# Performance work log

Hardware: AMD Instinct MI355X
Metric: run time of the kernel (lower is better)

Reference implementation:

```python
import jax, jax.numpy as jnp
import numpy as np

B, T, HID = 4, 2048, 2048
N_HEAD, N_KV, HD = 16, 2, 128
N_REP = N_HEAD // N_KV


def setup_inputs() -> dict:
    key = jax.random.key(0)
    ks = jax.random.split(key, 7)
    s = 0.02
    return {
        "x": jax.random.normal(ks[0], (B, T, HID), jnp.float32),
        "cos": jax.random.normal(ks[1], (T, 1, HD // 2), jnp.float32),
        "sin": jax.random.normal(ks[2], (T, 1, HD // 2), jnp.float32),
        "Wq": jax.random.normal(ks[3], (N_HEAD * HD, HID), jnp.float32) * s,
        "Wk": jax.random.normal(ks[4], (N_KV * HD, HID), jnp.float32) * s,
        "Wv": jax.random.normal(ks[5], (N_KV * HD, HID), jnp.float32) * s,
        "Wo": jax.random.normal(ks[6], (HID, HID), jnp.float32) * s,
    }


def _rope(x, cos, sin):
    # x: (B, T, H, HD); cos/sin: (T, 1, HD//2) broadcast over B and H
    x_r = x[..., 0::2]
    x_i = x[..., 1::2]
    out_r = x_r * cos - x_i * sin
    out_i = x_r * sin + x_i * cos
    return jnp.stack([out_r, out_i], axis=-1).reshape(x.shape)


def _rms_norm(x):
    eps = jnp.finfo(x.dtype).eps
    var = jnp.mean(jnp.square(x), axis=-1, keepdims=True)
    return x * jax.lax.rsqrt(var + eps)


def reference(x, cos, sin, Wq, Wk, Wv, Wo):
    b, t, _ = x.shape
    q = (x @ Wq.T).reshape(b, t, N_HEAD, HD)
    k = (x @ Wk.T).reshape(b, t, N_KV, HD)
    v = (x @ Wv.T).reshape(b, t, N_KV, HD)
    q = _rms_norm(_rope(q, cos, sin))
    k = _rms_norm(_rope(k, cos, sin))
    # GQA without materializing repeated K/V: group q heads per kv head
    # q: (b, t, n_kv, n_rep, hd) -> (b, n_kv, n_rep, t, hd)
    q = q.reshape(b, t, N_KV, N_REP, HD).transpose(0, 2, 3, 1, 4)
    k = k.transpose(0, 2, 1, 3)  # (b, n_kv, t, hd)
    v = v.transpose(0, 2, 1, 3)
    scale = 1.0 / jnp.sqrt(jnp.asarray(HD, x.dtype))
    scores = jnp.einsum("bgrtd,bgsd->bgrts", q, k) * scale
    causal = jnp.tril(jnp.ones((t, t), dtype=bool))
    scores = jnp.where(causal, scores, jnp.asarray(-jnp.inf, scores.dtype))
    attn = jax.nn.softmax(scores, axis=-1)
    y = jnp.einsum("bgrts,bgsd->bgrtd", attn, v)
    # (b, n_kv, n_rep, t, hd) -> (b, t, n_head*hd)
    y = y.transpose(0, 3, 1, 2, 4).reshape(b, t, N_HEAD * HD)
    return y @ Wo.T
```

## Files before the change

### kernel.cpp

```cpp
#include <hip/hip_runtime.h>

#define B_    4
#define T_    2048
#define HID_  2048
#define NH_   16
#define NKV_  2
#define HD_   128
#define M_    (B_ * T_)
#define NQKV_ 2560

typedef __bf16 bf16x8 __attribute__((ext_vector_type(8)));
typedef float  f32x4  __attribute__((ext_vector_type(4)));

#define AS1 __attribute__((address_space(1)))
#define AS3 __attribute__((address_space(3)))

#if __has_builtin(__builtin_amdgcn_exp2f)
#define EXP2(x) __builtin_amdgcn_exp2f(x)
#else
#define EXP2(x) exp2f(x)
#endif

__device__ __forceinline__ void load_lds16(const void* g, void* l) {
  __builtin_amdgcn_global_load_lds((const AS1 unsigned int*)g,
                                   (AS3 unsigned int*)l, 16, 0, 0);
}

__device__ __forceinline__ unsigned short f2bf(float x) {
  union { float f; unsigned u; } a; a.f = x;
  unsigned r = a.u + 0x7fffu + ((a.u >> 16) & 1u);
  return (unsigned short)(r >> 16);
}
__device__ __forceinline__ float bf2f(unsigned h) {
  union { unsigned u; float f; } a; a.u = h << 16;
  return a.f;
}
__device__ __forceinline__ unsigned pk_rtz(float lo, float hi) {
  union { float f; unsigned u; } a, b; a.f = lo; b.f = hi;
  return (a.u >> 16) | (b.u & 0xffff0000u);
}

__global__ __launch_bounds__(256) void cast_bf16(const float* __restrict__ in,
                                                 unsigned short* __restrict__ out,
                                                 int n4) {
  int i = blockIdx.x * 256 + threadIdx.x;
  if (i >= n4) return;
  float4 v = ((const float4*)in)[i];
  ushort4 o;
  o.x = f2bf(v.x); o.y = f2bf(v.y); o.z = f2bf(v.z); o.w = f2bf(v.w);
  ((ushort4*)out)[i] = o;
}

__global__ __launch_bounds__(256) void cast_w(const float* __restrict__ Wq,
                                              const float* __restrict__ Wk,
                                              const float* __restrict__ Wv,
                                              unsigned short* __restrict__ out) {
  int i = blockIdx.x * 256 + threadIdx.x;
  const float* src; int j;
  if (i < 1048576)      { src = Wq; j = i; }
  else if (i < 1179648) { src = Wk; j = i - 1048576; }
  else                  { src = Wv; j = i - 1179648; }
  float4 v = ((const float4*)src)[j];
  ushort4 o;
  o.x = f2bf(v.x); o.y = f2bf(v.y); o.z = f2bf(v.z); o.w = f2bf(v.w);
  ((ushort4*)out)[i] = o;
}

template <int OUT_BF16>
__global__ __launch_bounds__(256) void gemm_bt(const unsigned short* __restrict__ A,
                                               const unsigned short* __restrict__ Bm,
                                               void* __restrict__ C,
                                               int M, int N, int K) {
  __shared__ __align__(16) unsigned short As[128 * 32];
  __shared__ __align__(16) unsigned short Bs[128 * 32];
  const int tid = threadIdx.x;
  const int w = tid >> 6, lane = tid & 63;
  const int m0 = blockIdx.y << 7, n0 = blockIdx.x << 7;
  const int c = lane & 15, grp = lane >> 4;
  const int lr = lane >> 2;
  const int su = (((lane & 3) ^ ((lr >> 1) & 3)) << 3);
  const int sw = (c >> 1) & 3;
  const int wm = (w & 1) << 6, wn = (w >> 1) << 6;
  f32x4 acc[4][4] = {};
  for (int k0 = 0; k0 < K; k0 += 32) {
    __syncthreads();
    {
      int r0 = w << 4;
      load_lds16(A + (size_t)(m0 + r0 + lr) * K + k0 + su, &As[r0 * 32]);
      load_lds16(A + (size_t)(m0 + 64 + r0 + lr) * K + k0 + su, &As[(64 + r0) * 32]);
      load_lds16(Bm + (size_t)(n0 + r0 + lr) * K + k0 + su, &Bs[r0 * 32]);
      load_lds16(Bm + (size_t)(n0 + 64 + r0 + lr) * K + k0 + su, &Bs[(64 + r0) * 32]);
    }
    __syncthreads();
    bf16x8 af[4], bf[4];
#pragma unroll
    for (int i = 0; i < 4; i++)
      af[i] = *(const bf16x8*)&As[(wm + i * 16 + c) * 32 + ((grp ^ sw) << 3)];
#pragma unroll
    for (int j = 0; j < 4; j++)
      bf[j] = *(const bf16x8*)&Bs[(wn + j * 16 + c) * 32 + ((grp ^ sw) << 3)];
#pragma unroll
    for (int i = 0; i < 4; i++)
#pragma unroll
      for (int j = 0; j < 4; j++)
        acc[i][j] = __builtin_amdgcn_mfma_f32_16x16x32_bf16(af[i], bf[j], acc[i][j], 0, 0, 0);
  }
#pragma unroll
  for (int i = 0; i < 4; i++)
#pragma unroll
    for (int j = 0; j < 4; j++)
#pragma unroll
      for (int r = 0; r < 4; r++) {
        int row = m0 + wm + i * 16 + grp * 4 + r;
        int col = n0 + wn + j * 16 + c;
        float v = acc[i][j][r];
        if (OUT_BF16) ((unsigned short*)C)[(size_t)row * N + col] = f2bf(v);
        else          ((float*)C)[(size_t)row * N + col] = v;
      }
}

__global__ __launch_bounds__(256) void rope_norm(const unsigned short* __restrict__ qkv,
                                                 const float* __restrict__ cosb,
                                                 const float* __restrict__ sinb,
                                                 unsigned short* __restrict__ qo,
                                                 unsigned short* __restrict__ ko,
                                                 unsigned short* __restrict__ vo) {
  const int m = blockIdx.x;
  const int b = m >> 11, t = m & 2047;
  const int w = threadIdx.x >> 6, lane = threadIdx.x & 63;
  const float cv = cosb[t * 64 + lane], sv = sinb[t * 64 + lane];
  const unsigned short* row = qkv + (size_t)m * NQKV_;
  const float QSCL = 0.08838834764831845f * 1.4426950408889634f;
  for (int hh = w; hh < 20; hh += 4) {
    if (hh < 18) {
      const int col0 = (hh < 16) ? hh * 128 : 2048 + (hh - 16) * 128;
      unsigned pr = *(const unsigned*)(row + col0 + 2 * lane);
      float xr = bf2f(pr & 0xffffu), xi = bf2f(pr >> 16);
      float orr = xr * cv - xi * sv;
      float oi  = xr * sv + xi * cv;
      float ss = orr * orr + oi * oi;
#pragma unroll
      for (int off = 1; off < 64; off <<= 1) ss += __shfl_xor(ss, off);
      float scl = rsqrtf(ss * (1.0f / 128.0f) + 1.1920929e-07f);
      if (hh < 16) {
        float s2 = scl * QSCL;
        unsigned out = (unsigned)f2bf(orr * s2) | ((unsigned)f2bf(oi * s2) << 16);
        *(unsigned*)(qo + (((size_t)(b * NH_ + hh)) * T_ + t) * HD_ + 2 * lane) = out;
      } else {
        unsigned out = (unsigned)f2bf(orr * scl) | ((unsigned)f2bf(oi * scl) << 16);
        *(unsigned*)(ko + (((size_t)(b * NKV_ + (hh - 16))) * T_ + t) * HD_ + 2 * lane) = out;
      }
    } else {
      const int gg = hh - 18;
      unsigned pr = *(const unsigned*)(row + 2304 + gg * 128 + 2 * lane);
      *(unsigned*)(vo + (((size_t)(b * NKV_ + gg)) * T_ + t) * HD_ + 2 * lane) = pr;
    }
  }
}

__global__ __launch_bounds__(256) void transpose_v(const unsigned short* __restrict__ v,
                                                   unsigned short* __restrict__ vt) {
  __shared__ unsigned short tile[64][65];
  const int bg = blockIdx.z;
  const int t0 = blockIdx.x << 6, h0 = blockIdx.y << 6;
  const unsigned short* src = v + (size_t)bg * T_ * HD_;
  unsigned short* dst = vt + (size_t)bg * T_ * HD_;
  const int tid = threadIdx.x;
  const int rr = tid >> 4, cc = (tid & 15) << 2;
  const int u = (cc >> 2) & 7;
  const int cp = (cc & 32) + 16 * (u & 1) + 4 * ((u >> 1) & 3);
#pragma unroll
  for (int it = 0; it < 4; it++) {
    int r = rr + it * 16;
    ushort4 d = *(const ushort4*)(src + (size_t)(t0 + r) * HD_ + h0 + cc);
    tile[r][cc + 0] = d.x; tile[r][cc + 1] = d.y;
    tile[r][cc + 2] = d.z; tile[r][cc + 3] = d.w;
  }
  __syncthreads();
#pragma unroll
  for (int it = 0; it < 4; it++) {
    int r = rr + it * 16;
    ushort4 d;
    d.x = tile[cp + 0][r]; d.y = tile[cp + 1][r];
    d.z = tile[cp + 2][r]; d.w = tile[cp + 3][r];
    *(ushort4*)(dst + (size_t)(h0 + r) * T_ + t0 + cc) = d;
  }
}

__global__ __launch_bounds__(256, 2) void flash_attn(const unsigned short* __restrict__ q,
                                                     const unsigned short* __restrict__ k,
                                                     const unsigned short* __restrict__ vt,
                                                     unsigned short* __restrict__ y) {
  __shared__ __align__(16) unsigned short Kb[2][8192];
  __shared__ __align__(16) unsigned short Vb[2][8192];
  const int tid = threadIdx.x;
  const int w = tid >> 6, lane = tid & 63;
  const int c = lane & 15, grp = lane >> 4;
  const int lr = lane >> 2;
  const int sw = (c >> 1) & 3;
  const int su = (((lane & 3) ^ ((lr >> 1) & 3)) << 3);
  const int t0 = (15 - (int)blockIdx.x) << 7;
  const int t0w = t0 + w * 32;
  const int hq = blockIdx.y, b = blockIdx.z, g = hq >> 3;
  const unsigned short* qbase = q + (((size_t)(b * NH_ + hq)) * T_ + t0) * HD_;
  const unsigned short* kbase = k + ((size_t)(b * NKV_ + g)) * T_ * HD_;
  const unsigned short* vtbase = vt + ((size_t)(b * NKV_ + g)) * HD_ * T_;

  bf16x8 qf[2][4];
#pragma unroll
  for (int ti = 0; ti < 2; ti++)
#pragma unroll
    for (int ks = 0; ks < 4; ks++)
      qf[ti][ks] = *(const bf16x8*)(qbase + (size_t)(w * 32 + ti * 16 + c) * HD_ + ks * 32 + grp * 8);

  f32x4 oacc[2][8] = {};
  float mrun[2], lrun[2];
  mrun[0] = mrun[1] = -__builtin_inff();
  lrun[0] = lrun[1] = 0.f;

  auto stage = [&](int s0, int bb) {
    const unsigned short* kp = kbase + (size_t)(s0 + w * 16 + lr) * HD_ + su;
#pragma unroll
    for (int dc = 0; dc < 4; dc++)
      load_lds16(kp + dc * 32, &Kb[bb][dc * 2048 + (w * 16) * 32]);
    const unsigned short* vp = vtbase + s0 + su;
#pragma unroll
    for (int ks = 0; ks < 2; ks++)
#pragma unroll
      for (int jj = 0; jj < 2; jj++)
        load_lds16(vp + (size_t)(w * 32 + jj * 16 + lr) * T_ + ks * 32,
                   &Vb[bb][ks * 4096 + (w * 32 + jj * 16) * 32]);
  };

  const int nch = (t0 >> 6) + 2;
  stage(0, 0);
  __syncthreads();
  for (int ic = 0; ic < nch; ic++) {
    const int s0 = ic << 6, bb = ic & 1;
    if (ic + 1 < nch) stage((ic + 1) << 6, bb ^ 1);
    if (s0 <= t0w + 31) {
      const unsigned short* Kc = Kb[bb];
      const unsigned short* Vc = Vb[bb];
      f32x4 st[2][4] = {};
#pragma unroll
      for (int s = 0; s < 4; s++)
#pragma unroll
        for (int kvt = 0; kvt < 4; kvt++) {
          bf16x8 ak = *(const bf16x8*)&Kc[s * 2048 + (kvt * 16 + c) * 32 + ((grp ^ sw) << 3)];
          st[0][kvt] = __builtin_amdgcn_mfma_f32_16x16x32_bf16(ak, qf[0][s], st[0][kvt], 0, 0, 0);
          st[1][kvt] = __builtin_amdgcn_mfma_f32_16x16x32_bf16(ak, qf[1][s], st[1][kvt], 0, 0, 0);
        }
      if (s0 + 63 > t0w) {
#pragma unroll
        for (int ti = 0; ti < 2; ti++)
#pragma unroll
          for (int kvt = 0; kvt < 4; kvt++)
#pragma unroll
            for (int r = 0; r < 4; r++) {
              int kv = s0 + kvt * 16 + grp * 4 + r;
              int qq = t0w + ti * 16 + c;
              if (kv > qq) st[ti][kvt][r] = -__builtin_inff();
            }
      }
      unsigned pkv[2][4][2];
#pragma unroll
      for (int ti = 0; ti < 2; ti++) {
        float rm = st[ti][0][0];
#pragma unroll
        for (int kvt = 0; kvt < 4; kvt++)
#pragma unroll
          for (int r = 0; r < 4; r++) rm = fmaxf(rm, st[ti][kvt][r]);
        rm = fmaxf(rm, __shfl_xor(rm, 16));
        rm = fmaxf(rm, __shfl_xor(rm, 32));
        float mnew = fmaxf(mrun[ti], rm);
        float alpha = EXP2(mrun[ti] - mnew);
        mrun[ti] = mnew;
        float rs = 0.f;
#pragma unroll
        for (int kvt = 0; kvt < 4; kvt++) {
          float p0 = EXP2(st[ti][kvt][0] - mnew);
          float p1 = EXP2(st[ti][kvt][1] - mnew);
          float p2 = EXP2(st[ti][kvt][2] - mnew);
          float p3 = EXP2(st[ti][kvt][3] - mnew);
          rs += (p0 + p1) + (p2 + p3);
          pkv[ti][kvt][0] = pk_rtz(p0, p1);
          pkv[ti][kvt][1] = pk_rtz(p2, p3);
        }
        rs += __shfl_xor(rs, 16);
        rs += __shfl_xor(rs, 32);
        lrun[ti] = lrun[ti] * alpha + rs;
#pragma unroll
        for (int hj = 0; hj < 8; hj++)
#pragma unroll
          for (int r = 0; r < 4; r++) oacc[ti][hj][r] *= alpha;
      }
#pragma unroll
      for (int s = 0; s < 2; s++) {
        union { int4 i; bf16x8 v; } pf0, pf1;
        pf0.i = make_int4(pkv[0][2 * s][0], pkv[0][2 * s][1], pkv[0][2 * s + 1][0], pkv[0][2 * s + 1][1]);
        pf1.i = make_int4(pkv[1][2 * s][0], pkv[1][2 * s][1], pkv[1][2 * s + 1][0], pkv[1][2 * s + 1][1]);
#pragma unroll
        for (int hj = 0; hj < 8; hj++) {
          union { int4 i; bf16x8 v; } av;
          av.i = *(const int4*)&Vc[s * 4096 + (hj * 16 + c) * 32 + ((grp ^ sw) << 3)];
          oacc[0][hj] = __builtin_amdgcn_mfma_f32_16x16x32_bf16(av.v, pf0.v, oacc[0][hj], 0, 0, 0);
          oacc[1][hj] = __builtin_amdgcn_mfma_f32_16x16x32_bf16(av.v, pf1.v, oacc[1][hj], 0, 0, 0);
        }
      }
    }
    __syncthreads();
  }

#pragma unroll
  for (int ti = 0; ti < 2; ti++) {
    float inv = 1.f / lrun[ti];
    int trow = t0 + w * 32 + ti * 16 + c;
#pragma unroll
    for (int hj = 0; hj < 8; hj++) {
      ushort4 o;
      o.x = f2bf(oacc[ti][hj][0] * inv);
      o.y = f2bf(oacc[ti][hj][1] * inv);
      o.z = f2bf(oacc[ti][hj][2] * inv);
      o.w = f2bf(oacc[ti][hj][3] * inv);
      *(ushort4*)&y[((size_t)(b * T_ + trow)) * HID_ + hq * HD_ + hj * 16 + grp * 4] = o;
    }
  }
}

extern "C" void kernel_launch(void* const* d_in, const int* in_sizes, int n_in,
                              void* d_out, int out_size, void* d_ws, size_t ws_size,
                              hipStream_t stream) {
  const float* x    = (const float*)d_in[0];
  const float* cosb = (const float*)d_in[1];
  const float* sinb = (const float*)d_in[2];
  const float* Wq   = (const float*)d_in[3];
  const float* Wk   = (const float*)d_in[4];
  const float* Wv   = (const float*)d_in[5];
  const float* Wo   = (const float*)d_in[6];
  float* out = (float*)d_out;

  char* ws = (char*)d_ws;
  size_t off = 0;
  auto take = [&](size_t elems) {
    unsigned short* p = (unsigned short*)(ws + off);
    off += ((elems * 2 + 255) & ~(size_t)255);
    return p;
  };
  unsigned short* xb   = take((size_t)M_ * HID_);
  unsigned short* wqkv = take((size_t)NQKV_ * HID_);
  unsigned short* wob  = take((size_t)HID_ * HID_);
  unsigned short* qkv  = take((size_t)M_ * NQKV_);
  unsigned short* qb   = take((size_t)B_ * NH_ * T_ * HD_);
  unsigned short* kb   = take((size_t)B_ * NKV_ * T_ * HD_);
  unsigned short* vb   = take((size_t)B_ * NKV_ * T_ * HD_);
  unsigned short* vtb  = take((size_t)B_ * NKV_ * T_ * HD_);
  unsigned short* yb   = take((size_t)M_ * HID_);
  (void)ws_size; (void)in_sizes; (void)n_in; (void)out_size;

  cast_bf16<<<16384, 256, 0, stream>>>(x, xb, 4194304);
  cast_w<<<5120, 256, 0, stream>>>(Wq, Wk, Wv, wqkv);
  cast_bf16<<<4096, 256, 0, stream>>>(Wo, wob, 1048576);

  gemm_bt<1><<<dim3(20, 64), 256, 0, stream>>>(xb, wqkv, qkv, M_, NQKV_, HID_);
  rope_norm<<<8192, 256, 0, stream>>>(qkv, cosb, sinb, qb, kb, vb);
  transpose_v<<<dim3(32, 2, 8), 256, 0, stream>>>(vb, vtb);
  flash_attn<<<dim3(16, 16, 4), 256, 0, stream>>>(qb, kb, vtb, yb);
  gemm_bt<0><<<dim3(16, 64), 256, 0, stream>>>(yb, wob, out, M_, HID_, HID_);
}
```

Before: 546.3 us.

## Load V directly from global, drop V LDS staging, remap block schedule

```diff
diff --git a/kernel.cpp b/kernel.cpp
--- a/kernel.cpp
+++ b/kernel.cpp
@@ -187,24 +187,32 @@
   }
 }
 
-__global__ __launch_bounds__(256, 2) void flash_attn(const unsigned short* __restrict__ q,
+__global__ __launch_bounds__(256, 4) void flash_attn(const unsigned short* __restrict__ q,
                                                      const unsigned short* __restrict__ k,
                                                      const unsigned short* __restrict__ vt,
                                                      unsigned short* __restrict__ y) {
   __shared__ __align__(16) unsigned short Kb[2][8192];
-  __shared__ __align__(16) unsigned short Vb[2][8192];
   const int tid = threadIdx.x;
   const int w = tid >> 6, lane = tid & 63;
   const int c = lane & 15, grp = lane >> 4;
   const int lr = lane >> 2;
   const int sw = (c >> 1) & 3;
   const int su = (((lane & 3) ^ ((lr >> 1) & 3)) << 3);
-  const int t0 = (15 - (int)blockIdx.x) << 7;
+
+  const int idx = blockIdx.x;
+  const int j = idx >> 8;
+  const int u = idx & 15;
+  const int v = (idx >> 4) & 15;
+  const int tp = (u + 2 * (j >> 1)) & 15;
+  const int tile_i = (j & 1) ? tp : (15 - tp);
+  const int t0 = tile_i << 7;
+  const int hq = v, b = j, g = hq >> 3;
   const int t0w = t0 + w * 32;
-  const int hq = blockIdx.y, b = blockIdx.z, g = hq >> 3;
+
   const unsigned short* qbase = q + (((size_t)(b * NH_ + hq)) * T_ + t0) * HD_;
   const unsigned short* kbase = k + ((size_t)(b * NKV_ + g)) * T_ * HD_;
   const unsigned short* vtbase = vt + ((size_t)(b * NKV_ + g)) * HD_ * T_;
+  const unsigned short* vg = vtbase + (size_t)c * T_ + grp * 8;
 
   bf16x8 qf[2][4];
 #pragma unroll
@@ -223,13 +231,6 @@
 #pragma unroll
     for (int dc = 0; dc < 4; dc++)
       load_lds16(kp + dc * 32, &Kb[bb][dc * 2048 + (w * 16) * 32]);
-    const unsigned short* vp = vtbase + s0 + su;
-#pragma unroll
-    for (int ks = 0; ks < 2; ks++)
-#pragma unroll
-      for (int jj = 0; jj < 2; jj++)
-        load_lds16(vp + (size_t)(w * 32 + jj * 16 + lr) * T_ + ks * 32,
-                   &Vb[bb][ks * 4096 + (w * 32 + jj * 16) * 32]);
   };
 
   const int nch = (t0 >> 6) + 2;
@@ -240,7 +241,6 @@
     if (ic + 1 < nch) stage((ic + 1) << 6, bb ^ 1);
     if (s0 <= t0w + 31) {
       const unsigned short* Kc = Kb[bb];
-      const unsigned short* Vc = Vb[bb];
       f32x4 st[2][4] = {};
 #pragma unroll
       for (int s = 0; s < 4; s++)
@@ -296,15 +296,17 @@
       }
 #pragma unroll
       for (int s = 0; s < 2; s++) {
+        union { int4 i; bf16x8 v; } av[8];
+#pragma unroll
+        for (int hj = 0; hj < 8; hj++)
+          av[hj].i = *(const int4*)(vg + (size_t)(hj * 16) * T_ + s0 + s * 32);
         union { int4 i; bf16x8 v; } pf0, pf1;
         pf0.i = make_int4(pkv[0][2 * s][0], pkv[0][2 * s][1], pkv[0][2 * s + 1][0], pkv[0][2 * s + 1][1]);
         pf1.i = make_int4(pkv[1][2 * s][0], pkv[1][2 * s][1], pkv[1][2 * s + 1][0], pkv[1][2 * s + 1][1]);
 #pragma unroll
         for (int hj = 0; hj < 8; hj++) {
-          union { int4 i; bf16x8 v; } av;
-          av.i = *(const int4*)&Vc[s * 4096 + (hj * 16 + c) * 32 + ((grp ^ sw) << 3)];
-          oacc[0][hj] = __builtin_amdgcn_mfma_f32_16x16x32_bf16(av.v, pf0.v, oacc[0][hj], 0, 0, 0);
-          oacc[1][hj] = __builtin_amdgcn_mfma_f32_16x16x32_bf16(av.v, pf1.v, oacc[1][hj], 0, 0, 0);
+          oacc[0][hj] = __builtin_amdgcn_mfma_f32_16x16x32_bf16(av[hj].v, pf0.v, oacc[0][hj], 0, 0, 0);
+          oacc[1][hj] = __builtin_amdgcn_mfma_f32_16x16x32_bf16(av[hj].v, pf1.v, oacc[1][hj], 0, 0, 0);
         }
       }
     }
@@ -364,6 +366,6 @@
   gemm_bt<1><<<dim3(20, 64), 256, 0, stream>>>(xb, wqkv, qkv, M_, NQKV_, HID_);
   rope_norm<<<8192, 256, 0, stream>>>(qkv, cosb, sinb, qb, kb, vb);
   transpose_v<<<dim3(32, 2, 8), 256, 0, stream>>>(vb, vtb);
-  flash_attn<<<dim3(16, 16, 4), 256, 0, stream>>>(qb, kb, vtb, yb);
+  flash_attn<<<dim3(1024), 256, 0, stream>>>(qb, kb, vtb, yb);
   gemm_bt<0><<<dim3(16, 64), 256, 0, stream>>>(yb, wob, out, M_, HID_, HID_);
 }
```

New measurement: 768.1 us. 40.6% more time.

## Pair causal tiles per block, skip small rescales, raise MFMA priority

Applied to the files above, without the earlier changes.

```diff
diff --git a/kernel.cpp b/kernel.cpp
--- a/kernel.cpp
+++ b/kernel.cpp
@@ -199,24 +199,15 @@
   const int lr = lane >> 2;
   const int sw = (c >> 1) & 3;
   const int su = (((lane & 3) ^ ((lr >> 1) & 3)) << 3);
-  const int t0 = (15 - (int)blockIdx.x) << 7;
-  const int t0w = t0 + w * 32;
-  const int hq = blockIdx.y, b = blockIdx.z, g = hq >> 3;
-  const unsigned short* qbase = q + (((size_t)(b * NH_ + hq)) * T_ + t0) * HD_;
-  const unsigned short* kbase = k + ((size_t)(b * NKV_ + g)) * T_ * HD_;
+
+  const int idx = blockIdx.x;
+  const int p  = idx & 7;
+  const int hq = (idx >> 3) & 15;
+  const int b  = idx >> 7;
+  const int g  = hq >> 3;
+
+  const unsigned short* kbase  = k  + ((size_t)(b * NKV_ + g)) * T_ * HD_;
   const unsigned short* vtbase = vt + ((size_t)(b * NKV_ + g)) * HD_ * T_;
-
-  bf16x8 qf[2][4];
-#pragma unroll
-  for (int ti = 0; ti < 2; ti++)
-#pragma unroll
-    for (int ks = 0; ks < 4; ks++)
-      qf[ti][ks] = *(const bf16x8*)(qbase + (size_t)(w * 32 + ti * 16 + c) * HD_ + ks * 32 + grp * 8);
-
-  f32x4 oacc[2][8] = {};
-  float mrun[2], lrun[2];
-  mrun[0] = mrun[1] = -__builtin_inff();
-  lrun[0] = lrun[1] = 0.f;
 
   auto stage = [&](int s0, int bb) {
     const unsigned short* kp = kbase + (size_t)(s0 + w * 16 + lr) * HD_ + su;
@@ -232,97 +223,124 @@
                    &Vb[bb][ks * 4096 + (w * 32 + jj * 16) * 32]);
   };
 
-  const int nch = (t0 >> 6) + 2;
-  stage(0, 0);
-  __syncthreads();
-  for (int ic = 0; ic < nch; ic++) {
-    const int s0 = ic << 6, bb = ic & 1;
-    if (ic + 1 < nch) stage((ic + 1) << 6, bb ^ 1);
-    if (s0 <= t0w + 31) {
-      const unsigned short* Kc = Kb[bb];
-      const unsigned short* Vc = Vb[bb];
-      f32x4 st[2][4] = {};
-#pragma unroll
-      for (int s = 0; s < 4; s++)
-#pragma unroll
-        for (int kvt = 0; kvt < 4; kvt++) {
-          bf16x8 ak = *(const bf16x8*)&Kc[s * 2048 + (kvt * 16 + c) * 32 + ((grp ^ sw) << 3)];
-          st[0][kvt] = __builtin_amdgcn_mfma_f32_16x16x32_bf16(ak, qf[0][s], st[0][kvt], 0, 0, 0);
-          st[1][kvt] = __builtin_amdgcn_mfma_f32_16x16x32_bf16(ak, qf[1][s], st[1][kvt], 0, 0, 0);
+  for (int ph = 0; ph < 2; ph++) {
+    const int tile = ph ? p : (15 - p);
+    const int t0 = tile << 7;
+    const int t0w = t0 + w * 32;
+    const unsigned short* qbase = q + (((size_t)(b * NH_ + hq)) * T_ + t0) * HD_;
+
+    bf16x8 qf[2][4];
+#pragma unroll
+    for (int ti = 0; ti < 2; ti++)
+#pragma unroll
+      for (int ks = 0; ks < 4; ks++)
+        qf[ti][ks] = *(const bf16x8*)(qbase + (size_t)(w * 32 + ti * 16 + c) * HD_ + ks * 32 + grp * 8);
+
+    f32x4 oacc[2][8] = {};
+    float mrun[2], lrun[2];
+    mrun[0] = mrun[1] = -__builtin_inff();
+    lrun[0] = lrun[1] = 0.f;
+
+    const int nch = (t0 >> 6) + 2;
+    stage(0, 0);
+    __syncthreads();
+    for (int ic = 0; ic < nch; ic++) {
+      const int s0 = ic << 6, bb = ic & 1;
+      if (ic + 1 < nch) stage((ic + 1) << 6, bb ^ 1);
+      if (s0 <= t0w + 31) {
+        const unsigned short* Kc = Kb[bb];
+        const unsigned short* Vc = Vb[bb];
+        f32x4 st[2][4] = {};
+        __builtin_amdgcn_s_setprio(1);
+#pragma unroll
+        for (int s = 0; s < 4; s++)
+#pragma unroll
+          for (int kvt = 0; kvt < 4; kvt++) {
+            bf16x8 ak = *(const bf16x8*)&Kc[s * 2048 + (kvt * 16 + c) * 32 + ((grp ^ sw) << 3)];
+            st[0][kvt] = __builtin_amdgcn_mfma_f32_16x16x32_bf16(ak, qf[0][s], st[0][kvt], 0, 0, 0);
+            st[1][kvt] = __builtin_amdgcn_mfma_f32_16x16x32_bf16(ak, qf[1][s], st[1][kvt], 0, 0, 0);
+          }
+        __builtin_amdgcn_s_setprio(0);
+        if (s0 + 63 > t0w) {
+#pragma unroll
+          for (int ti = 0; ti < 2; ti++)
+#pragma unroll
+            for (int kvt = 0; kvt < 4; kvt++)
+#pragma unroll
+              for (int r = 0; r < 4; r++) {
+                int kv = s0 + kvt * 16 + grp * 4 + r;
+                int qq = t0w + ti * 16 + c;
+                if (kv > qq) st[ti][kvt][r] = -__builtin_inff();
+              }
         }
-      if (s0 + 63 > t0w) {
-#pragma unroll
-        for (int ti = 0; ti < 2; ti++)
+        unsigned pkv[2][4][2];
+#pragma unroll
+        for (int ti = 0; ti < 2; ti++) {
+          float rm = st[ti][0][0];
 #pragma unroll
           for (int kvt = 0; kvt < 4; kvt++)
 #pragma unroll
-            for (int r = 0; r < 4; r++) {
-              int kv = s0 + kvt * 16 + grp * 4 + r;
-              int qq = t0w + ti * 16 + c;
-              if (kv > qq) st[ti][kvt][r] = -__builtin_inff();
-            }
+            for (int r = 0; r < 4; r++) rm = fmaxf(rm, st[ti][kvt][r]);
+          rm = fmaxf(rm, __shfl_xor(rm, 16));
+          rm = fmaxf(rm, __shfl_xor(rm, 32));
+          if (!__all(rm <= mrun[ti] + 8.f)) {
+            float mnew = fmaxf(mrun[ti], rm);
+            float alpha = EXP2(mrun[ti] - mnew);
+            mrun[ti] = mnew;
+            lrun[ti] *= alpha;
+#pragma unroll
+            for (int hj = 0; hj < 8; hj++)
+#pragma unroll
+              for (int r = 0; r < 4; r++) oacc[ti][hj][r] *= alpha;
+          }
+          const float m0 = mrun[ti];
+          float rs = 0.f;
+#pragma unroll
+          for (int kvt = 0; kvt < 4; kvt++) {
+            float p0 = EXP2(st[ti][kvt][0] - m0);
+            float p1 = EXP2(st[ti][kvt][1] - m0);
+            float p2 = EXP2(st[ti][kvt][2] - m0);
+            float p3 = EXP2(st[ti][kvt][3] - m0);
+            rs += (p0 + p1) + (p2 + p3);
+            pkv[ti][kvt][0] = pk_rtz(p0, p1);
+            pkv[ti][kvt][1] = pk_rtz(p2, p3);
+          }
+          rs += __shfl_xor(rs, 16);
+          rs += __shfl_xor(rs, 32);
+          lrun[ti] += rs;
+        }
+        __builtin_amdgcn_s_setprio(1);
+#pragma unroll
+        for (int s = 0; s < 2; s++) {
+          union { int4 i; bf16x8 v; } pf0, pf1;
+          pf0.i = make_int4(pkv[0][2 * s][0], pkv[0][2 * s][1], pkv[0][2 * s + 1][0], pkv[0][2 * s + 1][1]);
+          pf1.i = make_int4(pkv[1][2 * s][0], pkv[1][2 * s][1], pkv[1][2 * s + 1][0], pkv[1][2 * s + 1][1]);
+#pragma unroll
+          for (int hj = 0; hj < 8; hj++) {
+            union { int4 i; bf16x8 v; } av;
+            av.i = *(const int4*)&Vc[s * 4096 + (hj * 16 + c) * 32 + ((grp ^ sw) << 3)];
+            oacc[0][hj] = __builtin_amdgcn_mfma_f32_16x16x32_bf16(av.v, pf0.v, oacc[0][hj], 0, 0, 0);
+            oacc[1][hj] = __builtin_amdgcn_mfma_f32_16x16x32_bf16(av.v, pf1.v, oacc[1][hj], 0, 0, 0);
+          }
+        }
+        __builtin_amdgcn_s_setprio(0);
       }
-      unsigned pkv[2][4][2];
-#pragma unroll
-      for (int ti = 0; ti < 2; ti++) {
-        float rm = st[ti][0][0];
-#pragma unroll
-        for (int kvt = 0; kvt < 4; kvt++)
-#pragma unroll
-          for (int r = 0; r < 4; r++) rm = fmaxf(rm, st[ti][kvt][r]);
-        rm = fmaxf(rm, __shfl_xor(rm, 16));
-        rm = fmaxf(rm, __shfl_xor(rm, 32));
-        float mnew = fmaxf(mrun[ti], rm);
-        float alpha = EXP2(mrun[ti] - mnew);
-        mrun[ti] = mnew;
-        float rs = 0.f;
-#pragma unroll
-        for (int kvt = 0; kvt < 4; kvt++) {
-          float p0 = EXP2(st[ti][kvt][0] - mnew);
-          float p1 = EXP2(st[ti][kvt][1] - mnew);
-          float p2 = EXP2(st[ti][kvt][2] - mnew);
-          float p3 = EXP2(st[ti][kvt][3] - mnew);
-          rs += (p0 + p1) + (p2 + p3);
-          pkv[ti][kvt][0] = pk_rtz(p0, p1);
-          pkv[ti][kvt][1] = pk_rtz(p2, p3);
-        }
-        rs += __shfl_xor(rs, 16);
-        rs += __shfl_xor(rs, 32);
-        lrun[ti] = lrun[ti] * alpha + rs;
-#pragma unroll
-        for (int hj = 0; hj < 8; hj++)
-#pragma unroll
-          for (int r = 0; r < 4; r++) oacc[ti][hj][r] *= alpha;
+      __syncthreads();
+    }
+
+#pragma unroll
+    for (int ti = 0; ti < 2; ti++) {
+      float inv = 1.f / lrun[ti];
+      int trow = t0 + w * 32 + ti * 16 + c;
+#pragma unroll
+      for (int hj = 0; hj < 8; hj++) {
+        ushort4 o;
+        o.x = f2bf(oacc[ti][hj][0] * inv);
+        o.y = f2bf(oacc[ti][hj][1] * inv);
+        o.z = f2bf(oacc[ti][hj][2] * inv);
+        o.w = f2bf(oacc[ti][hj][3] * inv);
+        *(ushort4*)&y[((size_t)(b * T_ + trow)) * HID_ + hq * HD_ + hj * 16 + grp * 4] = o;
       }
-#pragma unroll
-      for (int s = 0; s < 2; s++) {
-        union { int4 i; bf16x8 v; } pf0, pf1;
-        pf0.i = make_int4(pkv[0][2 * s][0], pkv[0][2 * s][1], pkv[0][2 * s + 1][0], pkv[0][2 * s + 1][1]);
-        pf1.i = make_int4(pkv[1][2 * s][0], pkv[1][2 * s][1], pkv[1][2 * s + 1][0], pkv[1][2 * s + 1][1]);
-#pragma unroll
-        for (int hj = 0; hj < 8; hj++) {
-          union { int4 i; bf16x8 v; } av;
-          av.i = *(const int4*)&Vc[s * 4096 + (hj * 16 + c) * 32 + ((grp ^ sw) << 3)];
-          oacc[0][hj] = __builtin_amdgcn_mfma_f32_16x16x32_bf16(av.v, pf0.v, oacc[0][hj], 0, 0, 0);
-          oacc[1][hj] = __builtin_amdgcn_mfma_f32_16x16x32_bf16(av.v, pf1.v, oacc[1][hj], 0, 0, 0);
-        }
-      }
-    }
-    __syncthreads();
-  }
-
-#pragma unroll
-  for (int ti = 0; ti < 2; ti++) {
-    float inv = 1.f / lrun[ti];
-    int trow = t0 + w * 32 + ti * 16 + c;
-#pragma unroll
-    for (int hj = 0; hj < 8; hj++) {
-      ushort4 o;
-      o.x = f2bf(oacc[ti][hj][0] * inv);
-      o.y = f2bf(oacc[ti][hj][1] * inv);
-      o.z = f2bf(oacc[ti][hj][2] * inv);
-      o.w = f2bf(oacc[ti][hj][3] * inv);
-      *(ushort4*)&y[((size_t)(b * T_ + trow)) * HID_ + hq * HD_ + hj * 16 + grp * 4] = o;
     }
   }
 }
@@ -364,6 +382,6 @@
   gemm_bt<1><<<dim3(20, 64), 256, 0, stream>>>(xb, wqkv, qkv, M_, NQKV_, HID_);
   rope_norm<<<8192, 256, 0, stream>>>(qkv, cosb, sinb, qb, kb, vb);
   transpose_v<<<dim3(32, 2, 8), 256, 0, stream>>>(vb, vtb);
-  flash_attn<<<dim3(16, 16, 4), 256, 0, stream>>>(qb, kb, vtb, yb);
+  flash_attn<<<dim3(512), 256, 0, stream>>>(qb, kb, vtb, yb);
   gemm_bt<0><<<dim3(16, 64), 256, 0, stream>>>(yb, wob, out, M_, HID_, HID_);
 }
```

After: 478.3 us. -12.4%, faster.
